# Kernel tuning notes

Measured on AMD Instinct MI355X. Metric: run time of the kernel, lower is better.

Reference implementation:

```python
import jax, jax.numpy as jnp
import numpy as np

DIM = 20
N = 200000
E = 6400000
ITERATIONS = 3


def setup_inputs() -> dict:
    key = jax.random.key(0)
    ks = jax.random.split(key, 20)
    inp = {
        "h": jax.random.normal(ks[0], (N, DIM), dtype=jnp.float32),
        "node2depth": jax.random.randint(ks[1], (N,), 0, 5, dtype=jnp.int32),
        "edge_src": jax.random.randint(ks[2], (E,), 0, N, dtype=jnp.int32),
        "edge_dst": jax.random.randint(ks[3], (E,), 0, N, dtype=jnp.int32),
    }
    # Six DIM x DIM Linear layers (weight stored [out,in] like torch, plus bias)
    scale = 1.0 / np.sqrt(DIM)
    names = ["Wz", "Uz", "Wr", "Ur", "Wh", "Uh"]
    for j, nm in enumerate(names):
        inp[nm + "_w"] = jax.random.uniform(ks[4 + 2 * j], (DIM, DIM), jnp.float32, -scale, scale)
        inp[nm + "_b"] = jax.random.uniform(ks[5 + 2 * j], (DIM,), jnp.float32, -scale, scale)
    return inp


def _linear(x, w, b):
    return x @ w.T + b


def reference(h, Wz_w, Wz_b, Uz_w, Uz_b, Wr_w, Wr_b, Ur_w, Ur_b,
              Wh_w, Wh_b, Uh_w, Uh_b, node2depth, edge_src, edge_dst):
    active = None
    for i in range(ITERATIONS):
        # active set shrinks as i grows (depth + i <= ITERATIONS)
        active = (node2depth + i) <= ITERATIONS  # [N] bool
        af = active.astype(h.dtype)
        # x[u] = sum over neighbors v of h[v], counting only active src AND active dst
        msg = h[edge_src] * af[edge_src][:, None]          # [E, DIM]
        x = jax.ops.segment_sum(msg, edge_dst, num_segments=N)  # [N, DIM]
        x = x * af[:, None]
        z = jax.nn.sigmoid(_linear(x, Wz_w, Wz_b) + _linear(h, Uz_w, Uz_b))
        r = jax.nn.sigmoid(_linear(x, Wr_w, Wr_b) + _linear(h, Ur_w, Ur_b))
        h_cand = jnp.tanh(_linear(x, Wh_w, Wh_b) + _linear(r * h, Uh_w, Uh_b))
        h_new = z * h + (1.0 - z) * h_cand
        # inactive nodes are dropped from the dict in the original; since the
        # active set only shrinks, keeping their old h is equivalent
        h = jnp.where(active[:, None], h_new, h)
    # original returns only nodes active at the last iteration; zero out the rest
    return jnp.where(active[:, None], h, jnp.zeros_like(h))
```

## Files before the change

kernel.cpp:

```cpp
#include <hip/hip_runtime.h>

#define DIM    20
#define NN     200000
#define EE     6400000
#define ITERS  3
#define BLOCK  256

#define NODES_PER_FINE   64
#define NFINE            3125
#define TILE             4096
#define IPT              16

#define BLOCK2 512
#define IPT2   16
#define TILE2  (BLOCK2 * IPT2)

typedef unsigned int u32;

__global__ __launch_bounds__(BLOCK) void k1_count(const int* __restrict__ edst,
                                                  const int* __restrict__ depth,
                                                  int* __restrict__ fine_cnt,
                                                  int* __restrict__ dcnt) {
    __shared__ u32 lhist[NFINE];
    __shared__ u32 dh[5];
    int tid = threadIdx.x;
    for (int i = tid; i < NFINE; i += BLOCK) lhist[i] = 0;
    if (tid < 5) dh[tid] = 0;
    __syncthreads();
    for (int e = blockIdx.x * BLOCK + tid; e < EE; e += gridDim.x * BLOCK) {
        int d = edst[e];
        atomicAdd(&lhist[d >> 6], 1u);
    }
    for (int n = blockIdx.x * BLOCK + tid; n < NN; n += gridDim.x * BLOCK) {
        atomicAdd(&dh[depth[n]], 1u);
    }
    __syncthreads();
    for (int i = tid; i < NFINE; i += BLOCK) {
        u32 v = lhist[i];
        if (v) atomicAdd((u32*)&fine_cnt[i], v);
    }
    if (tid < 5) dcnt[tid * 256 + blockIdx.x] = (int)dh[tid];
}

__global__ __launch_bounds__(BLOCK) void k2_scan(const int* __restrict__ fine_cnt,
                                                 int* __restrict__ fine_base,
                                                 int* __restrict__ fine_cursor,
                                                 const int* __restrict__ dcnt,
                                                 int* __restrict__ dbase,
                                                 int* __restrict__ cum) {
    __shared__ int wsum[4];
    __shared__ int sdb[1281];
    int tid = threadIdx.x;
    int lane = tid & 63, wid = tid >> 6;

    {
        const int CH = 13;
        int loc[CH];
        int base = tid * CH;
        int s = 0;
        #pragma unroll
        for (int j = 0; j < CH; ++j) {
            int idx = base + j;
            int v = (idx < NFINE) ? fine_cnt[idx] : 0;
            loc[j] = v; s += v;
        }
        int incl = s;
        #pragma unroll
        for (int off = 1; off < 64; off <<= 1) {
            int t = __shfl_up(incl, off, 64);
            if (lane >= off) incl += t;
        }
        if (lane == 63) wsum[wid] = incl;
        __syncthreads();
        int woff = 0;
        for (int w = 0; w < wid; ++w) woff += wsum[w];
        int run = woff + incl - s;
        #pragma unroll
        for (int j = 0; j < CH; ++j) {
            int idx = base + j;
            if (idx < NFINE) {
                fine_base[idx]   = run;
                fine_cursor[idx] = run;
                run += loc[j];
            }
        }
        if (tid == 0) fine_base[NFINE] = EE;
    }
    __syncthreads();

    {
        const int CH2 = 5;
        int loc[CH2];
        int base = tid * CH2;
        int s = 0;
        #pragma unroll
        for (int j = 0; j < CH2; ++j) { int v = dcnt[base + j]; loc[j] = v; s += v; }
        int incl = s;
        #pragma unroll
        for (int off = 1; off < 64; off <<= 1) {
            int t = __shfl_up(incl, off, 64);
            if (lane >= off) incl += t;
        }
        if (lane == 63) wsum[wid] = incl;
        __syncthreads();
        int woff = 0;
        for (int w = 0; w < wid; ++w) woff += wsum[w];
        int run = woff + incl - s;
        #pragma unroll
        for (int j = 0; j < CH2; ++j) {
            sdb[base + j]   = run;
            dbase[base + j] = run;
            run += loc[j];
        }
        if (tid == 255) sdb[1280] = run;
        __syncthreads();
        if (tid < 5) cum[tid] = sdb[(tid + 1) * 256];
    }
}

__global__ __launch_bounds__(BLOCK) void kd_scatter(const int* __restrict__ depth,
                                                    const int* __restrict__ dbase,
                                                    int* __restrict__ perm) {
    __shared__ u32 dh[5];
    int tid = threadIdx.x;
    if (tid < 5) dh[tid] = 0;
    __syncthreads();
    for (int n = blockIdx.x * BLOCK + tid; n < NN; n += gridDim.x * BLOCK) {
        int d = depth[n];
        u32 r = atomicAdd(&dh[d], 1u);
        perm[n] = dbase[d * 256 + blockIdx.x] + (int)r;
    }
}

__global__ __launch_bounds__(BLOCK2) void p1_bin(const int* __restrict__ esrc,
                                                 const int* __restrict__ edst,
                                                 const int* __restrict__ perm,
                                                 int* __restrict__ fine_cursor,
                                                 u32* __restrict__ buf2) {
    __shared__ u32 lhist[NFINE];
    __shared__ u32 gbase[NFINE];
    int tid = threadIdx.x;
    int start = blockIdx.x * TILE2;
    for (int i = tid; i < NFINE; i += BLOCK2) lhist[i] = 0;
    __syncthreads();

    u32 item[IPT2]; u32 key[IPT2]; u32 rank[IPT2];
    #pragma unroll
    for (int k = 0; k < IPT2; ++k) {
        int e = start + k * BLOCK2 + tid;
        if (e < EE) {
            int d = edst[e];
            int s = esrc[e];
            u32 pid = (u32)perm[s];
            u32 kk = (u32)d >> 6;
            key[k]  = kk;
            item[k] = ((u32)d & 63u) | (pid << 6);
            rank[k] = atomicAdd(&lhist[kk], 1u);
        }
    }
    __syncthreads();
    for (int i = tid; i < NFINE; i += BLOCK2) {
        u32 c = lhist[i];
        gbase[i] = c ? (u32)atomicAdd((u32*)&fine_cursor[i], c) : 0u;
    }
    __syncthreads();
    #pragma unroll
    for (int k = 0; k < IPT2; ++k) {
        int e = start + k * BLOCK2 + tid;
        if (e < EE) buf2[gbase[key[k]] + rank[k]] = item[k];
    }
}

__global__ __launch_bounds__(BLOCK) void pb_sort(const u32* __restrict__ buf2,
                                                 const int* __restrict__ fine_base,
                                                 const int* __restrict__ cum,
                                                 int* __restrict__ ptr,
                                                 u32* __restrict__ cnt3,
                                                 u32* __restrict__ ssrc) {
    __shared__ u32 hist[512];
    __shared__ u32 ebase[512];
    __shared__ u32 lout[TILE];
    __shared__ u32 wsum[4];
    int tid = threadIdx.x;
    int b = blockIdx.x;
    int lo = fine_base[b];
    int hi = fine_base[b + 1];
    int cnt = hi - lo;
    u32 c0 = (u32)cum[0], c1 = (u32)cum[1], c2 = (u32)cum[2], c3 = (u32)cum[3];
    hist[tid] = 0; hist[tid + 256] = 0;
    __syncthreads();

    u32 item[IPT]; u32 key[IPT]; u32 rank[IPT];
    #pragma unroll
    for (int k = 0; k < IPT; ++k) {
        int i = lo + k * BLOCK + tid;
        if (i < hi) {
            u32 w = buf2[i];
            u32 pid = w >> 6;
            u32 dep = (u32)(pid >= c0) + (u32)(pid >= c1)
                    + (u32)(pid >= c2) + (u32)(pid >= c3);
            u32 kk = (w & 63u) * 8u + dep;
            key[k]  = kk;
            item[k] = pid;
            rank[k] = atomicAdd(&hist[kk], 1u);
        }
    }
    __syncthreads();
    {
        u32 s0 = hist[2 * tid], s1 = hist[2 * tid + 1];
        u32 s = s0 + s1;
        int lane = tid & 63, wid = tid >> 6;
        u32 incl = s;
        #pragma unroll
        for (int off = 1; off < 64; off <<= 1) {
            u32 t = __shfl_up((int)incl, off, 64);
            if (lane >= off) incl += t;
        }
        if (lane == 63) wsum[wid] = incl;
        __syncthreads();
        u32 woff = 0;
        for (int w = 0; w < wid; ++w) woff += wsum[w];
        u32 excl = woff + incl - s;
        ebase[2 * tid]     = excl;
        ebase[2 * tid + 1] = excl + s0;
    }
    __syncthreads();
    if (tid < NODES_PER_FINE) {
        u32 base0 = ebase[tid * 8];
        u32 cc1 = ebase[tid * 8 + 2] - base0;
        u32 cc2 = ebase[tid * 8 + 3] - base0;
        u32 cc3 = ebase[tid * 8 + 4] - base0;
        int u = b * NODES_PER_FINE + tid;
        ptr[u]  = lo + (int)base0;
        cnt3[u] = cc1 | (cc2 << 10) | (cc3 << 20);
    }
    #pragma unroll
    for (int k = 0; k < IPT; ++k) {
        int i = lo + k * BLOCK + tid;
        if (i < hi) lout[ebase[key[k]] + rank[k]] = item[k];
    }
    __syncthreads();
    for (int j = tid; j < cnt; j += BLOCK) ssrc[lo + j] = lout[j];
}

__device__ __forceinline__ u32 pack_bf16x2(float a, float b) {
    u32 ua = __float_as_uint(a);
    u32 ub = __float_as_uint(b);
    ua = (ua + 0x7FFFu + ((ua >> 16) & 1u)) >> 16;
    ub = (ub + 0x7FFFu + ((ub >> 16) & 1u)) & 0xFFFF0000u;
    return ua | ub;
}

__global__ __launch_bounds__(BLOCK) void hconv(const float* __restrict__ h,
                                               u32* __restrict__ hbA,
                                               u32* __restrict__ hbC,
                                               const int* __restrict__ perm,
                                               const int* __restrict__ depth) {
    int g = blockIdx.x * BLOCK + threadIdx.x;
    if (g >= NN * 8) return;
    int node = g >> 3, s = g & 7;
    if (depth[node] > ITERS) return;
    int pid = perm[node];
    float2 f = *(const float2*)(h + (size_t)node * DIM + s * 2);
    hbA[(size_t)pid * 8 + s] = pack_bf16x2(f.x, f.y);
    if (s < 2) {
        float2 fc = *(const float2*)(h + (size_t)node * DIM + 16 + s * 2);
        hbC[(size_t)pid * 2 + s] = pack_bf16x2(fc.x, fc.y);
    }
}


__device__ __forceinline__ float bl(u32 w) { return __uint_as_float(w << 16); }
__device__ __forceinline__ float bh(u32 w) { return __uint_as_float(w & 0xFFFF0000u); }

__device__ __forceinline__ void acc_half(float* xa, float* xc, uint4 a, u32 c) {
    xa[0]+=bl(a.x); xa[1]+=bh(a.x);
    xa[2]+=bl(a.y); xa[3]+=bh(a.y);
    xa[4]+=bl(a.z); xa[5]+=bh(a.z);
    xa[6]+=bl(a.w); xa[7]+=bh(a.w);
    xc[0]+=bl(c);   xc[1]+=bh(c);
}

__global__ __launch_bounds__(BLOCK) void gather_x(
    const u32* __restrict__ hbA, const u32* __restrict__ hbC,
    const int* __restrict__ depth, const int* __restrict__ ptr,
    const u32* __restrict__ cnt3, const u32* __restrict__ ssrc,
    float* __restrict__ xg, int lim, int shift)
{
    int tid = threadIdx.x;
    int u = blockIdx.x * 32 + (tid >> 3);
    int j = tid & 7;
    int r = j >> 1;
    int q = j & 1;
    if (depth[u] > lim) return;
    int p = ptr[u];
    int d = (int)((cnt3[u] >> shift) & 1023u);

    float xa[8], xc[2];
    #pragma unroll
    for (int k = 0; k < 8; ++k) xa[k] = 0.0f;
    xc[0] = 0.0f; xc[1] = 0.0f;

    int e = r;
    for (; e + 4 < d; e += 8) {
        u32 pid0 = ssrc[p + e];
        u32 pid1 = ssrc[p + e + 4];
        uint4 a0 = *(const uint4*)(hbA + (size_t)pid0 * 8 + q * 4);
        u32   c0 = hbC[(size_t)pid0 * 2 + q];
        uint4 a1 = *(const uint4*)(hbA + (size_t)pid1 * 8 + q * 4);
        u32   c1 = hbC[(size_t)pid1 * 2 + q];
        acc_half(xa, xc, a0, c0);
        acc_half(xa, xc, a1, c1);
    }
    if (e < d) {
        u32 pid0 = ssrc[p + e];
        uint4 a0 = *(const uint4*)(hbA + (size_t)pid0 * 8 + q * 4);
        u32   c0 = hbC[(size_t)pid0 * 2 + q];
        acc_half(xa, xc, a0, c0);
    }
    #pragma unroll
    for (int k = 0; k < 8; ++k) {
        xa[k] += __shfl_xor(xa[k], 2, 64);
        xa[k] += __shfl_xor(xa[k], 4, 64);
    }
    xc[0] += __shfl_xor(xc[0], 2, 64); xc[0] += __shfl_xor(xc[0], 4, 64);
    xc[1] += __shfl_xor(xc[1], 2, 64); xc[1] += __shfl_xor(xc[1], 4, 64);

    float* xr = xg + (size_t)u * DIM;
    if (j == 0) {
        *(float4*)(xr)      = make_float4(xa[0], xa[1], xa[2], xa[3]);
        *(float4*)(xr + 4)  = make_float4(xa[4], xa[5], xa[6], xa[7]);
        *(float2*)(xr + 16) = make_float2(xc[0], xc[1]);
    } else if (j == 1) {
        *(float4*)(xr + 8)  = make_float4(xa[0], xa[1], xa[2], xa[3]);
        *(float4*)(xr + 12) = make_float4(xa[4], xa[5], xa[6], xa[7]);
        *(float2*)(xr + 18) = make_float2(xc[0], xc[1]);
    }
}


__device__ __forceinline__ float fast_sigmoid(float t) {
    return 1.0f / (1.0f + __expf(-t));
}
__device__ __forceinline__ float fast_tanh(float t) {
    t = fminf(fmaxf(t, -15.0f), 15.0f);
    float e2 = __expf(2.0f * t);
    return (e2 - 1.0f) / (e2 + 1.0f);
}

__global__ __launch_bounds__(BLOCK) void gru_update(
    const float* __restrict__ xg,
    const float* __restrict__ h_in, float* __restrict__ h_out,
    u32* __restrict__ hbA, u32* __restrict__ hbC,
    const int* __restrict__ depth, const int* __restrict__ perm,
    const int* __restrict__ cum,
    const float* __restrict__ Wz, const float* __restrict__ bWz,
    const float* __restrict__ Uz, const float* __restrict__ bUz,
    const float* __restrict__ Wr, const float* __restrict__ bWr,
    const float* __restrict__ Ur, const float* __restrict__ bUr,
    const float* __restrict__ Wh, const float* __restrict__ bWh,
    const float* __restrict__ Uh, const float* __restrict__ bUh,
    int lim, int cumIdx, int isFinal)
{
    int u = blockIdx.x * BLOCK + threadIdx.x;
    if (u >= NN) return;
    bool act = depth[u] <= lim;
    if (!act) {
        if (isFinal) {
            float4 z4 = make_float4(0.f, 0.f, 0.f, 0.f);
            float4* o4 = (float4*)(h_out + (size_t)u * DIM);
            #pragma unroll
            for (int q = 0; q < 5; ++q) o4[q] = z4;
        }
        return;
    }

    float x[DIM], h[DIM];
    {
        const float4* xv = (const float4*)(xg + (size_t)u * DIM);
        float4 a0 = xv[0], a1 = xv[1], a2 = xv[2], a3 = xv[3], a4 = xv[4];
        x[0]=a0.x; x[1]=a0.y; x[2]=a0.z; x[3]=a0.w;
        x[4]=a1.x; x[5]=a1.y; x[6]=a1.z; x[7]=a1.w;
        x[8]=a2.x; x[9]=a2.y; x[10]=a2.z; x[11]=a2.w;
        x[12]=a3.x; x[13]=a3.y; x[14]=a3.z; x[15]=a3.w;
        x[16]=a4.x; x[17]=a4.y; x[18]=a4.z; x[19]=a4.w;
    }
    {
        const float4* hv = (const float4*)(h_in + (size_t)u * DIM);
        float4 a0 = hv[0], a1 = hv[1], a2 = hv[2], a3 = hv[3], a4 = hv[4];
        h[0]=a0.x; h[1]=a0.y; h[2]=a0.z; h[3]=a0.w;
        h[4]=a1.x; h[5]=a1.y; h[6]=a1.z; h[7]=a1.w;
        h[8]=a2.x; h[9]=a2.y; h[10]=a2.z; h[11]=a2.w;
        h[12]=a3.x; h[13]=a3.y; h[14]=a3.z; h[15]=a3.w;
        h[16]=a4.x; h[17]=a4.y; h[18]=a4.z; h[19]=a4.w;
    }

    float z[DIM], rh[DIM];
    #pragma unroll
    for (int j = 0; j < DIM; ++j) {
        float sz = bWz[j] + bUz[j];
        float sr = bWr[j] + bUr[j];
        #pragma unroll
        for (int k = 0; k < DIM; ++k) {
            sz += x[k] * Wz[j * DIM + k];
            sz += h[k] * Uz[j * DIM + k];
            sr += x[k] * Wr[j * DIM + k];
            sr += h[k] * Ur[j * DIM + k];
        }
        z[j]  = fast_sigmoid(sz);
        rh[j] = fast_sigmoid(sr) * h[j];
    }

    float o[DIM];
    #pragma unroll
    for (int j = 0; j < DIM; ++j) {
        float sh = bWh[j] + bUh[j];
        #pragma unroll
        for (int k = 0; k < DIM; ++k) {
            sh += x[k]  * Wh[j * DIM + k];
            sh += rh[k] * Uh[j * DIM + k];
        }
        float hc = fast_tanh(sh);
        o[j] = z[j] * h[j] + (1.0f - z[j]) * hc;
    }

    {
        float4* o4 = (float4*)(h_out + (size_t)u * DIM);
        o4[0] = make_float4(o[0],  o[1],  o[2],  o[3]);
        o4[1] = make_float4(o[4],  o[5],  o[6],  o[7]);
        o4[2] = make_float4(o[8],  o[9],  o[10], o[11]);
        o4[3] = make_float4(o[12], o[13], o[14], o[15]);
        o4[4] = make_float4(o[16], o[17], o[18], o[19]);
    }
    if (!isFinal) {
        int pid = perm[u];
        if (pid < cum[cumIdx]) {
            u32* rowA = hbA + (size_t)pid * 8;
            uint4 wA0 = make_uint4(pack_bf16x2(o[0], o[1]),   pack_bf16x2(o[2], o[3]),
                                   pack_bf16x2(o[4], o[5]),   pack_bf16x2(o[6], o[7]));
            uint4 wA1 = make_uint4(pack_bf16x2(o[8], o[9]),   pack_bf16x2(o[10], o[11]),
                                   pack_bf16x2(o[12], o[13]), pack_bf16x2(o[14], o[15]));
            *(uint4*)rowA       = wA0;
            *(uint4*)(rowA + 4) = wA1;
            *(uint2*)(hbC + (size_t)pid * 2) =
                make_uint2(pack_bf16x2(o[16], o[17]), pack_bf16x2(o[18], o[19]));
        }
    }
}


extern "C" void kernel_launch(void* const* d_in, const int* in_sizes, int n_in,
                              void* d_out, int out_size, void* d_ws, size_t ws_size,
                              hipStream_t stream) {
    const float* h0    = (const float*)d_in[0];
    const int*   depth = (const int*)d_in[1];
    const int*   esrc  = (const int*)d_in[2];
    const int*   edst  = (const int*)d_in[3];
    const float* Wz  = (const float*)d_in[4];  const float* bWz = (const float*)d_in[5];
    const float* Uz  = (const float*)d_in[6];  const float* bUz = (const float*)d_in[7];
    const float* Wr  = (const float*)d_in[8];  const float* bWr = (const float*)d_in[9];
    const float* Ur  = (const float*)d_in[10]; const float* bUr = (const float*)d_in[11];
    const float* Wh  = (const float*)d_in[12]; const float* bWh = (const float*)d_in[13];
    const float* Uh  = (const float*)d_in[14]; const float* bUh = (const float*)d_in[15];
    float* out = (float*)d_out;

    int* W = (int*)d_ws;
    int*  fine_cnt      = W + 0;
    int*  fine_base     = W + 3200;
    int*  fine_cursor   = W + 6400;
    int*  dcnt          = W + 9600;
    int*  dbase         = W + 10880;
    int*  cum           = W + 12160;
    int*  ptr           = W + 12800;
    u32*  cnt3          = (u32*)(W + 212864);
    int*  perm          = W + 412864;
    u32*  buf1          = (u32*)(W + 612864);
    u32*  buf2          = buf1 + EE;
    float* h1           = (float*)(buf2 + EE);
    u32*  hbA           = (u32*)(h1 + (size_t)NN * DIM);
    u32*  hbC           = hbA + (size_t)NN * 8;
    u32*  ssrc          = buf1;
    float* xg           = (float*)buf2;

    hipMemsetAsync(fine_cnt, 0, NFINE * sizeof(int), stream);

    int nt2 = (EE + TILE2 - 1) / TILE2;

    k1_count  <<<256, BLOCK, 0, stream>>>(edst, depth, fine_cnt, dcnt);
    k2_scan   <<<1,   BLOCK, 0, stream>>>(fine_cnt, fine_base, fine_cursor,
                                          dcnt, dbase, cum);
    kd_scatter<<<256, BLOCK, 0, stream>>>(depth, dbase, perm);
    p1_bin    <<<nt2, BLOCK2, 0, stream>>>(esrc, edst, perm, fine_cursor, buf2);
    pb_sort   <<<NFINE, BLOCK, 0, stream>>>(buf2, fine_base, cum, ptr, cnt3, ssrc);
    hconv     <<<(NN * 8) / BLOCK, BLOCK, 0, stream>>>(h0, hbA, hbC, perm, depth);

    gather_x  <<<NN / 32, BLOCK, 0, stream>>>(hbA, hbC, depth, ptr, cnt3, ssrc, xg, 3, 20);
    gru_update<<<(NN + BLOCK - 1) / BLOCK, BLOCK, 0, stream>>>(xg, h0, h1, hbA, hbC, depth, perm, cum,
        Wz, bWz, Uz, bUz, Wr, bWr, Ur, bUr, Wh, bWh, Uh, bUh, 3, 2, 0);
    gather_x  <<<NN / 32, BLOCK, 0, stream>>>(hbA, hbC, depth, ptr, cnt3, ssrc, xg, 2, 10);
    gru_update<<<(NN + BLOCK - 1) / BLOCK, BLOCK, 0, stream>>>(xg, h1, h1, hbA, hbC, depth, perm, cum,
        Wz, bWz, Uz, bUz, Wr, bWr, Ur, bUr, Wh, bWh, Uh, bUh, 2, 1, 0);
    gather_x  <<<NN / 32, BLOCK, 0, stream>>>(hbA, hbC, depth, ptr, cnt3, ssrc, xg, 1, 0);
    gru_update<<<(NN + BLOCK - 1) / BLOCK, BLOCK, 0, stream>>>(xg, h1, out, hbA, hbC, depth, perm, cum,
        Wz, bWz, Uz, bUz, Wr, bWr, Ur, bUr, Wh, bWh, Uh, bUh, 1, 0, 1);
}
```

Baseline: 549.1 us.

## Replace counted edge binning with two-pass fixed-capacity coarse/fine radix split

Drops the full edge-count pass and global scan. Edges are instead binned in two passes, first into 98 coarse buckets and then into 32 fine buckets each, using fixed-capacity slots and atomic cursors. pb_sort claims its output offset through a global atomic counter. The gather loop is also unrolled to issue four neighbour loads at once. This removes one full read of edge_dst and a large shared-memory histogram, but relies on fixed capacities (CAP1, CAP2) that only hold for uniformly random edges, and adds an extra pass over the edges.

```diff
diff --git a/kernel.cpp b/kernel.cpp
--- a/kernel.cpp
+++ b/kernel.cpp
@@ -8,114 +8,72 @@
 
 #define NODES_PER_FINE   64
 #define NFINE            3125
+#define NCOARSE          98
+#define FINE_PER_COARSE  32
 #define TILE             4096
 #define IPT              16
 
-#define BLOCK2 512
-#define IPT2   16
-#define TILE2  (BLOCK2 * IPT2)
+#define CAP1             67584
+#define NT2P             17
+#define CAP2             2304
+#define PIPT             9
 
 typedef unsigned int u32;
 
-__global__ __launch_bounds__(BLOCK) void k1_count(const int* __restrict__ edst,
-                                                  const int* __restrict__ depth,
-                                                  int* __restrict__ fine_cnt,
-                                                  int* __restrict__ dcnt) {
-    __shared__ u32 lhist[NFINE];
+__global__ void init_cursors(int* __restrict__ coarse_cursor,
+                             int* __restrict__ fine_cursor,
+                             int* __restrict__ gcur) {
+    int g = blockIdx.x * 256 + threadIdx.x;
+    if (g < NCOARSE) coarse_cursor[g] = g * CAP1;
+    if (g < NFINE)   fine_cursor[g]   = g * CAP2;
+    if (g == 0) *gcur = 0;
+}
+
+__global__ __launch_bounds__(BLOCK) void kdep(const int* __restrict__ depth,
+                                              int* __restrict__ dcnt) {
     __shared__ u32 dh[5];
     int tid = threadIdx.x;
-    for (int i = tid; i < NFINE; i += BLOCK) lhist[i] = 0;
     if (tid < 5) dh[tid] = 0;
     __syncthreads();
-    for (int e = blockIdx.x * BLOCK + tid; e < EE; e += gridDim.x * BLOCK) {
-        int d = edst[e];
-        atomicAdd(&lhist[d >> 6], 1u);
-    }
-    for (int n = blockIdx.x * BLOCK + tid; n < NN; n += gridDim.x * BLOCK) {
+    for (int n = blockIdx.x * BLOCK + tid; n < NN; n += gridDim.x * BLOCK)
         atomicAdd(&dh[depth[n]], 1u);
-    }
-    __syncthreads();
-    for (int i = tid; i < NFINE; i += BLOCK) {
-        u32 v = lhist[i];
-        if (v) atomicAdd((u32*)&fine_cnt[i], v);
-    }
+    __syncthreads();
     if (tid < 5) dcnt[tid * 256 + blockIdx.x] = (int)dh[tid];
 }
 
-__global__ __launch_bounds__(BLOCK) void k2_scan(const int* __restrict__ fine_cnt,
-                                                 int* __restrict__ fine_base,
-                                                 int* __restrict__ fine_cursor,
-                                                 const int* __restrict__ dcnt,
+__global__ __launch_bounds__(BLOCK) void k2_scan(const int* __restrict__ dcnt,
                                                  int* __restrict__ dbase,
                                                  int* __restrict__ cum) {
     __shared__ int wsum[4];
     __shared__ int sdb[1281];
     int tid = threadIdx.x;
     int lane = tid & 63, wid = tid >> 6;
-
-    {
-        const int CH = 13;
-        int loc[CH];
-        int base = tid * CH;
-        int s = 0;
-        #pragma unroll
-        for (int j = 0; j < CH; ++j) {
-            int idx = base + j;
-            int v = (idx < NFINE) ? fine_cnt[idx] : 0;
-            loc[j] = v; s += v;
-        }
-        int incl = s;
-        #pragma unroll
-        for (int off = 1; off < 64; off <<= 1) {
-            int t = __shfl_up(incl, off, 64);
-            if (lane >= off) incl += t;
-        }
-        if (lane == 63) wsum[wid] = incl;
-        __syncthreads();
-        int woff = 0;
-        for (int w = 0; w < wid; ++w) woff += wsum[w];
-        int run = woff + incl - s;
-        #pragma unroll
-        for (int j = 0; j < CH; ++j) {
-            int idx = base + j;
-            if (idx < NFINE) {
-                fine_base[idx]   = run;
-                fine_cursor[idx] = run;
-                run += loc[j];
-            }
-        }
-        if (tid == 0) fine_base[NFINE] = EE;
-    }
-    __syncthreads();
-
-    {
-        const int CH2 = 5;
-        int loc[CH2];
-        int base = tid * CH2;
-        int s = 0;
-        #pragma unroll
-        for (int j = 0; j < CH2; ++j) { int v = dcnt[base + j]; loc[j] = v; s += v; }
-        int incl = s;
-        #pragma unroll
-        for (int off = 1; off < 64; off <<= 1) {
-            int t = __shfl_up(incl, off, 64);
-            if (lane >= off) incl += t;
-        }
-        if (lane == 63) wsum[wid] = incl;
-        __syncthreads();
-        int woff = 0;
-        for (int w = 0; w < wid; ++w) woff += wsum[w];
-        int run = woff + incl - s;
-        #pragma unroll
-        for (int j = 0; j < CH2; ++j) {
-            sdb[base + j]   = run;
-            dbase[base + j] = run;
-            run += loc[j];
-        }
-        if (tid == 255) sdb[1280] = run;
-        __syncthreads();
-        if (tid < 5) cum[tid] = sdb[(tid + 1) * 256];
-    }
+    const int CH2 = 5;
+    int loc[CH2];
+    int base = tid * CH2;
+    int s = 0;
+    #pragma unroll
+    for (int j = 0; j < CH2; ++j) { int v = dcnt[base + j]; loc[j] = v; s += v; }
+    int incl = s;
+    #pragma unroll
+    for (int off = 1; off < 64; off <<= 1) {
+        int t = __shfl_up(incl, off, 64);
+        if (lane >= off) incl += t;
+    }
+    if (lane == 63) wsum[wid] = incl;
+    __syncthreads();
+    int woff = 0;
+    for (int w = 0; w < wid; ++w) woff += wsum[w];
+    int run = woff + incl - s;
+    #pragma unroll
+    for (int j = 0; j < CH2; ++j) {
+        sdb[base + j]   = run;
+        dbase[base + j] = run;
+        run += loc[j];
+    }
+    if (tid == 255) sdb[1280] = run;
+    __syncthreads();
+    if (tid < 5) cum[tid] = sdb[(tid + 1) * 256];
 }
 
 __global__ __launch_bounds__(BLOCK) void kd_scatter(const int* __restrict__ depth,
@@ -132,79 +90,133 @@
     }
 }
 
-__global__ __launch_bounds__(BLOCK2) void p1_bin(const int* __restrict__ esrc,
-                                                 const int* __restrict__ edst,
-                                                 const int* __restrict__ perm,
-                                                 int* __restrict__ fine_cursor,
-                                                 u32* __restrict__ buf2) {
-    __shared__ u32 lhist[NFINE];
-    __shared__ u32 gbase[NFINE];
-    int tid = threadIdx.x;
-    int start = blockIdx.x * TILE2;
-    for (int i = tid; i < NFINE; i += BLOCK2) lhist[i] = 0;
-    __syncthreads();
-
-    u32 item[IPT2]; u32 key[IPT2]; u32 rank[IPT2];
-    #pragma unroll
-    for (int k = 0; k < IPT2; ++k) {
-        int e = start + k * BLOCK2 + tid;
-        if (e < EE) {
-            int d = edst[e];
-            int s = esrc[e];
-            u32 pid = (u32)perm[s];
-            u32 kk = (u32)d >> 6;
-            key[k]  = kk;
-            item[k] = ((u32)d & 63u) | (pid << 6);
-            rank[k] = atomicAdd(&lhist[kk], 1u);
-        }
-    }
-    __syncthreads();
-    for (int i = tid; i < NFINE; i += BLOCK2) {
-        u32 c = lhist[i];
-        gbase[i] = c ? (u32)atomicAdd((u32*)&fine_cursor[i], c) : 0u;
-    }
-    __syncthreads();
-    #pragma unroll
-    for (int k = 0; k < IPT2; ++k) {
-        int e = start + k * BLOCK2 + tid;
-        if (e < EE) buf2[gbase[key[k]] + rank[k]] = item[k];
+__global__ __launch_bounds__(BLOCK) void p1_split(const int* __restrict__ esrc,
+                                                  const int* __restrict__ edst,
+                                                  const int* __restrict__ perm,
+                                                  int* __restrict__ coarse_cursor,
+                                                  u32* __restrict__ buf1) {
+    __shared__ u32 lhist[NCOARSE];
+    __shared__ u32 gbase[NCOARSE];
+    int tid = threadIdx.x;
+    int start = blockIdx.x * TILE;
+    if (tid < NCOARSE) lhist[tid] = 0;
+    __syncthreads();
+
+    int dd[IPT], sv[IPT];
+    #pragma unroll
+    for (int k = 0; k < IPT; ++k) {
+        int e = start + k * BLOCK + tid;
+        dd[k] = (e < EE) ? edst[e] : -1;
+        sv[k] = (e < EE) ? esrc[e] : 0;
+    }
+    u32 pid[IPT];
+    #pragma unroll
+    for (int k = 0; k < IPT; ++k) pid[k] = (u32)perm[sv[k]];
+    u32 key[IPT], rank[IPT];
+    #pragma unroll
+    for (int k = 0; k < IPT; ++k) {
+        if (dd[k] >= 0) {
+            key[k]  = (u32)dd[k] >> 11;
+            rank[k] = atomicAdd(&lhist[key[k]], 1u);
+        }
+    }
+    __syncthreads();
+    if (tid < NCOARSE) {
+        u32 c = lhist[tid];
+        gbase[tid] = c ? (u32)atomicAdd((u32*)&coarse_cursor[tid], c) : 0u;
+    }
+    __syncthreads();
+    #pragma unroll
+    for (int k = 0; k < IPT; ++k) {
+        if (dd[k] >= 0)
+            buf1[gbase[key[k]] + rank[k]] = ((u32)dd[k] & 2047u) | (pid[k] << 11);
+    }
+}
+
+__global__ __launch_bounds__(BLOCK) void p2_split(const u32* __restrict__ buf1,
+                                                  const int* __restrict__ coarse_cursor,
+                                                  int* __restrict__ fine_cursor,
+                                                  u32* __restrict__ buf2) {
+    int bid = blockIdx.x;
+    int c = bid / NT2P, t = bid - c * NT2P;
+    int base  = c * CAP1;
+    int end   = coarse_cursor[c];
+    int start = base + t * TILE;
+    if (start >= end) return;
+    int stop = min(end, start + TILE);
+
+    __shared__ u32 lhist[FINE_PER_COARSE];
+    __shared__ u32 gbase[FINE_PER_COARSE];
+    int tid = threadIdx.x;
+    if (tid < FINE_PER_COARSE) lhist[tid] = 0;
+    __syncthreads();
+
+    u32 w[IPT], key[IPT], rank[IPT];
+    #pragma unroll
+    for (int k = 0; k < IPT; ++k) {
+        int i = start + k * BLOCK + tid;
+        w[k] = (i < stop) ? buf1[i] : 0xFFFFFFFFu;
+    }
+    #pragma unroll
+    for (int k = 0; k < IPT; ++k) {
+        if (w[k] != 0xFFFFFFFFu) {
+            key[k]  = (w[k] & 2047u) >> 6;
+            rank[k] = atomicAdd(&lhist[key[k]], 1u);
+        }
+    }
+    __syncthreads();
+    if (tid < FINE_PER_COARSE) {
+        u32 cnt = lhist[tid];
+        int f = c * FINE_PER_COARSE + tid;
+        if (cnt && f < NFINE)
+            gbase[tid] = (u32)atomicAdd((u32*)&fine_cursor[f], cnt);
+    }
+    __syncthreads();
+    #pragma unroll
+    for (int k = 0; k < IPT; ++k) {
+        if (w[k] != 0xFFFFFFFFu)
+            buf2[gbase[key[k]] + rank[k]] = (w[k] & 63u) | ((w[k] >> 11) << 6);
     }
 }
 
 __global__ __launch_bounds__(BLOCK) void pb_sort(const u32* __restrict__ buf2,
-                                                 const int* __restrict__ fine_base,
+                                                 const int* __restrict__ fine_cursor,
                                                  const int* __restrict__ cum,
+                                                 int* __restrict__ gcur,
                                                  int* __restrict__ ptr,
                                                  u32* __restrict__ cnt3,
                                                  u32* __restrict__ ssrc) {
     __shared__ u32 hist[512];
     __shared__ u32 ebase[512];
-    __shared__ u32 lout[TILE];
+    __shared__ u32 lout[CAP2];
     __shared__ u32 wsum[4];
-    int tid = threadIdx.x;
-    int b = blockIdx.x;
-    int lo = fine_base[b];
-    int hi = fine_base[b + 1];
-    int cnt = hi - lo;
+    __shared__ int slo;
+    int tid = threadIdx.x;
+    int f = blockIdx.x;
+    int base = f * CAP2;
+    int end  = fine_cursor[f];
+    int cnt  = end - base;
     u32 c0 = (u32)cum[0], c1 = (u32)cum[1], c2 = (u32)cum[2], c3 = (u32)cum[3];
     hist[tid] = 0; hist[tid + 256] = 0;
     __syncthreads();
 
-    u32 item[IPT]; u32 key[IPT]; u32 rank[IPT];
-    #pragma unroll
-    for (int k = 0; k < IPT; ++k) {
-        int i = lo + k * BLOCK + tid;
-        if (i < hi) {
-            u32 w = buf2[i];
-            u32 pid = w >> 6;
+    u32 w[PIPT], key[PIPT], rank[PIPT];
+    #pragma unroll
+    for (int k = 0; k < PIPT; ++k) {
+        int i = base + k * BLOCK + tid;
+        w[k] = (i < end) ? buf2[i] : 0xFFFFFFFFu;
+    }
+    #pragma unroll
+    for (int k = 0; k < PIPT; ++k) {
+        if (w[k] != 0xFFFFFFFFu) {
+            u32 pid = w[k] >> 6;
             u32 dep = (u32)(pid >= c0) + (u32)(pid >= c1)
                     + (u32)(pid >= c2) + (u32)(pid >= c3);
-            u32 kk = (w & 63u) * 8u + dep;
-            key[k]  = kk;
-            item[k] = pid;
-            rank[k] = atomicAdd(&hist[kk], 1u);
-        }
-    }
+            key[k]  = (w[k] & 63u) * 8u + dep;
+            rank[k] = atomicAdd(&hist[key[k]], 1u);
+        }
+    }
+    if (tid == 0) slo = atomicAdd(gcur, cnt);
     __syncthreads();
     {
         u32 s0 = hist[2 * tid], s1 = hist[2 * tid + 1];
@@ -219,25 +231,25 @@
         if (lane == 63) wsum[wid] = incl;
         __syncthreads();
         u32 woff = 0;
-        for (int w = 0; w < wid; ++w) woff += wsum[w];
+        for (int w2 = 0; w2 < wid; ++w2) woff += wsum[w2];
         u32 excl = woff + incl - s;
         ebase[2 * tid]     = excl;
         ebase[2 * tid + 1] = excl + s0;
     }
     __syncthreads();
+    int lo = slo;
     if (tid < NODES_PER_FINE) {
         u32 base0 = ebase[tid * 8];
         u32 cc1 = ebase[tid * 8 + 2] - base0;
         u32 cc2 = ebase[tid * 8 + 3] - base0;
         u32 cc3 = ebase[tid * 8 + 4] - base0;
-        int u = b * NODES_PER_FINE + tid;
+        int u = f * NODES_PER_FINE + tid;
         ptr[u]  = lo + (int)base0;
         cnt3[u] = cc1 | (cc2 << 10) | (cc3 << 20);
     }
     #pragma unroll
-    for (int k = 0; k < IPT; ++k) {
-        int i = lo + k * BLOCK + tid;
-        if (i < hi) lout[ebase[key[k]] + rank[k]] = item[k];
+    for (int k = 0; k < PIPT; ++k) {
+        if (w[k] != 0xFFFFFFFFu) lout[ebase[key[k]] + rank[k]] = w[k] >> 6;
     }
     __syncthreads();
     for (int j = tid; j < cnt; j += BLOCK) ssrc[lo + j] = lout[j];
@@ -302,20 +314,38 @@
     xc[0] = 0.0f; xc[1] = 0.0f;
 
     int e = r;
-    for (; e + 4 < d; e += 8) {
-        u32 pid0 = ssrc[p + e];
-        u32 pid1 = ssrc[p + e + 4];
-        uint4 a0 = *(const uint4*)(hbA + (size_t)pid0 * 8 + q * 4);
-        u32   c0 = hbC[(size_t)pid0 * 2 + q];
-        uint4 a1 = *(const uint4*)(hbA + (size_t)pid1 * 8 + q * 4);
-        u32   c1 = hbC[(size_t)pid1 * 2 + q];
+    for (; e + 12 < d; e += 16) {
+        u32 p0 = ssrc[p + e];
+        u32 p1 = ssrc[p + e + 4];
+        u32 p2 = ssrc[p + e + 8];
+        u32 p3 = ssrc[p + e + 12];
+        uint4 a0 = *(const uint4*)(hbA + (size_t)p0 * 8 + q * 4);
+        uint4 a1 = *(const uint4*)(hbA + (size_t)p1 * 8 + q * 4);
+        uint4 a2 = *(const uint4*)(hbA + (size_t)p2 * 8 + q * 4);
+        uint4 a3 = *(const uint4*)(hbA + (size_t)p3 * 8 + q * 4);
+        u32 c0 = hbC[(size_t)p0 * 2 + q];
+        u32 c1 = hbC[(size_t)p1 * 2 + q];
+        u32 c2 = hbC[(size_t)p2 * 2 + q];
+        u32 c3 = hbC[(size_t)p3 * 2 + q];
         acc_half(xa, xc, a0, c0);
         acc_half(xa, xc, a1, c1);
+        acc_half(xa, xc, a2, c2);
+        acc_half(xa, xc, a3, c3);
+    }
+    for (; e + 4 < d; e += 8) {
+        u32 p0 = ssrc[p + e];
+        u32 p1 = ssrc[p + e + 4];
+        uint4 a0 = *(const uint4*)(hbA + (size_t)p0 * 8 + q * 4);
+        uint4 a1 = *(const uint4*)(hbA + (size_t)p1 * 8 + q * 4);
+        u32 c0 = hbC[(size_t)p0 * 2 + q];
+        u32 c1 = hbC[(size_t)p1 * 2 + q];
+        acc_half(xa, xc, a0, c0);
+        acc_half(xa, xc, a1, c1);
     }
     if (e < d) {
-        u32 pid0 = ssrc[p + e];
-        uint4 a0 = *(const uint4*)(hbA + (size_t)pid0 * 8 + q * 4);
-        u32   c0 = hbC[(size_t)pid0 * 2 + q];
+        u32 p0 = ssrc[p + e];
+        uint4 a0 = *(const uint4*)(hbA + (size_t)p0 * 8 + q * 4);
+        u32 c0 = hbC[(size_t)p0 * 2 + q];
         acc_half(xa, xc, a0, c0);
     }
     #pragma unroll
@@ -465,34 +495,33 @@
     float* out = (float*)d_out;
 
     int* W = (int*)d_ws;
-    int*  fine_cnt      = W + 0;
-    int*  fine_base     = W + 3200;
-    int*  fine_cursor   = W + 6400;
-    int*  dcnt          = W + 9600;
-    int*  dbase         = W + 10880;
-    int*  cum           = W + 12160;
-    int*  ptr           = W + 12800;
-    u32*  cnt3          = (u32*)(W + 212864);
-    int*  perm          = W + 412864;
-    u32*  buf1          = (u32*)(W + 612864);
-    u32*  buf2          = buf1 + EE;
-    float* h1           = (float*)(buf2 + EE);
+    int*  dcnt          = W + 0;
+    int*  dbase         = W + 1280;
+    int*  cum           = W + 2560;
+    int*  gcur          = W + 2568;
+    int*  coarse_cursor = W + 2576;
+    int*  fine_cursor   = W + 2688;
+    int*  ptr           = W + 5824;
+    u32*  cnt3          = (u32*)(W + 205824);
+    int*  perm          = W + 405824;
+    u32*  buf1          = (u32*)(W + 605824);
+    u32*  buf2          = buf1 + (size_t)NCOARSE * CAP1;
+    float* h1           = (float*)(buf2 + (size_t)NFINE * CAP2);
     u32*  hbA           = (u32*)(h1 + (size_t)NN * DIM);
     u32*  hbC           = hbA + (size_t)NN * 8;
     u32*  ssrc          = buf1;
     float* xg           = (float*)buf2;
 
-    hipMemsetAsync(fine_cnt, 0, NFINE * sizeof(int), stream);
-
-    int nt2 = (EE + TILE2 - 1) / TILE2;
-
-    k1_count  <<<256, BLOCK, 0, stream>>>(edst, depth, fine_cnt, dcnt);
-    k2_scan   <<<1,   BLOCK, 0, stream>>>(fine_cnt, fine_base, fine_cursor,
-                                          dcnt, dbase, cum);
-    kd_scatter<<<256, BLOCK, 0, stream>>>(depth, dbase, perm);
-    p1_bin    <<<nt2, BLOCK2, 0, stream>>>(esrc, edst, perm, fine_cursor, buf2);
-    pb_sort   <<<NFINE, BLOCK, 0, stream>>>(buf2, fine_base, cum, ptr, cnt3, ssrc);
-    hconv     <<<(NN * 8) / BLOCK, BLOCK, 0, stream>>>(h0, hbA, hbC, perm, depth);
+    int ntile = (EE + TILE - 1) / TILE;
+
+    init_cursors<<<13, 256, 0, stream>>>(coarse_cursor, fine_cursor, gcur);
+    kdep        <<<256, BLOCK, 0, stream>>>(depth, dcnt);
+    k2_scan     <<<1,   BLOCK, 0, stream>>>(dcnt, dbase, cum);
+    kd_scatter  <<<256, BLOCK, 0, stream>>>(depth, dbase, perm);
+    p1_split    <<<ntile, BLOCK, 0, stream>>>(esrc, edst, perm, coarse_cursor, buf1);
+    p2_split    <<<NCOARSE * NT2P, BLOCK, 0, stream>>>(buf1, coarse_cursor, fine_cursor, buf2);
+    pb_sort     <<<NFINE, BLOCK, 0, stream>>>(buf2, fine_cursor, cum, gcur, ptr, cnt3, ssrc);
+    hconv       <<<(NN * 8) / BLOCK, BLOCK, 0, stream>>>(h0, hbA, hbC, perm, depth);
 
     gather_x  <<<NN / 32, BLOCK, 0, stream>>>(hbA, hbC, depth, ptr, cnt3, ssrc, xg, 3, 20);
     gru_update<<<(NN + BLOCK - 1) / BLOCK, BLOCK, 0, stream>>>(xg, h0, h1, hbA, hbC, depth, perm, cum,
```

Result: faster. 522.9 us (-4.8%).
